# Optimization experiments

Measured on AMD Instinct MI355X. Metric: run time of the kernel, lower is better.

Reference implementation:

```python
import jax, jax.numpy as jnp
import numpy as np

EMBED_DIM = 1024
NUM_HEADS = 16
HEAD_DIM = EMBED_DIM // NUM_HEADS


def setup_inputs() -> dict:
    key = jax.random.key(0)
    k_x, k_wqkv, k_bqkv, k_wp, k_bp = jax.random.split(key, 5)
    B, N, C = 4, 2048, EMBED_DIM
    bound_qkv = 1.0 / np.sqrt(C)
    bound_p = 1.0 / np.sqrt(C)
    return {
        "x": jax.random.normal(k_x, (B, N, C), dtype=jnp.float32),
        # nn.Linear stores weight as [out, in]; we keep that layout and use x @ W.T
        "w_qkv": jax.random.uniform(k_wqkv, (3 * C, C), jnp.float32, -bound_qkv, bound_qkv),
        "b_qkv": jax.random.uniform(k_bqkv, (3 * C,), jnp.float32, -bound_qkv, bound_qkv),
        "w_proj": jax.random.uniform(k_wp, (C, C), jnp.float32, -bound_p, bound_p),
        "b_proj": jax.random.uniform(k_bp, (C,), jnp.float32, -bound_p, bound_p),
    }


def reference(x, w_qkv, b_qkv, w_proj, b_proj):
    B, N, C = x.shape
    H, D = NUM_HEADS, HEAD_DIM
    qkv = x @ w_qkv.T + b_qkv                      # [B, N, 3C]
    qkv = qkv.reshape(B, N, 3, H, D)
    q = qkv[:, :, 0].transpose(0, 2, 1, 3)          # [B, H, N, D]
    k = qkv[:, :, 1].transpose(0, 2, 1, 3)
    v = qkv[:, :, 2].transpose(0, 2, 1, 3)
    scale = jnp.asarray(D, x.dtype) ** -0.5
    attn = jnp.einsum('bhqd,bhkd->bhqk', q, k) * scale  # [B, H, N, N]
    attn = jax.nn.softmax(attn, axis=-1)
    out = jnp.einsum('bhqk,bhkd->bhqd', attn, v)        # [B, H, N, D]
    out = out.transpose(0, 2, 1, 3).reshape(B, N, C)
    return out @ w_proj.T + b_proj
```

## Files before the change

kernel.cpp:

```cpp
#include <hip/hip_runtime.h>

typedef unsigned short u16;
typedef __attribute__((ext_vector_type(8))) short short8;
typedef __attribute__((ext_vector_type(4))) short s16x4;
typedef __attribute__((ext_vector_type(8))) _Float16 half8;
typedef __attribute__((ext_vector_type(4))) float f32x4;
typedef __attribute__((ext_vector_type(16))) float f32x16;
typedef __attribute__((ext_vector_type(4))) unsigned int u32x4;

#define DEVI static __device__ __forceinline__

static constexpr int B_ = 4, N_ = 2048, C_ = 1024, H_ = 16, D_ = 64;
static constexpr int M_ = B_ * N_;
static constexpr int C3 = 3072;

DEVI u16 f2h(float f) {
  _Float16 h = (_Float16)f;
  return __builtin_bit_cast(u16, h);
}

DEVI unsigned pk2h(float lo, float hi) {
  return __builtin_bit_cast(unsigned, __builtin_amdgcn_cvt_pkrtz(lo, hi));
}

DEVI void gload_lds16(const void* g, void* lds) {
  __builtin_amdgcn_global_load_lds(
      (const __attribute__((address_space(1))) unsigned int*)g,
      (__attribute__((address_space(3))) unsigned int*)lds, 16, 0, 0);
}

__global__ __launch_bounds__(256) void f32_to_f16(const float* __restrict__ src,
                                                  u16* __restrict__ dst, int n8) {
  int idx = blockIdx.x * 256 + threadIdx.x;
  if (idx >= n8) return;
  const float* s = src + (size_t)idx * 8;
  f32x4 f0 = *(const f32x4*)s;
  f32x4 f1 = *(const f32x4*)(s + 4);
  short8 o;
#pragma unroll
  for (int j = 0; j < 8; ++j) o[j] = (short)f2h(j < 4 ? f0[j] : f1[j - 4]);
  *(short8*)(dst + (size_t)idx * 8) = o;
}

template <bool OUT_F16>
__global__ __launch_bounds__(256) void gemm_bt(const u16* __restrict__ A,
                                               const u16* __restrict__ Bm,
                                               const float* __restrict__ bias,
                                               void* __restrict__ outp, int Nout) {
  __shared__ u16 As[128 * 32];
  __shared__ u16 Bs[128 * 32];
  const int tid = threadIdx.x;
  const int w = tid >> 6, l = tid & 63;
  const int wr = w >> 1, wc = w & 1;
  const int l15 = l & 15, lg = l >> 4;
  const int nx = gridDim.x;
  int bid = blockIdx.y * nx + blockIdx.x;
  int cpx = (nx * gridDim.y) >> 3;
  int swz = (bid & 7) * cpx + (bid >> 3);
  int bx = swz % nx, by = swz / nx;
  const u16* Ab = A + (size_t)(bx * 128) * C_;
  const u16* Bb = Bm + (size_t)(by * 128) * C_;
  const int arow = tid >> 2, ac8 = (tid & 3) * 8;
  f32x4 acc[4][4];
#pragma unroll
  for (int m = 0; m < 4; ++m)
#pragma unroll
    for (int n = 0; n < 4; ++n) acc[m][n] = (f32x4){0.f, 0.f, 0.f, 0.f};

  for (int kt = 0; kt < C_; kt += 32) {
    __syncthreads();
#pragma unroll
    for (int i = 0; i < 2; ++i) {
      gload_lds16(Ab + (size_t)(i * 64 + arow) * C_ + kt + ac8,
                  (char*)As + (i * 64 + w * 16) * 64);
      gload_lds16(Bb + (size_t)(i * 64 + arow) * C_ + kt + ac8,
                  (char*)Bs + (i * 64 + w * 16) * 64);
    }
    __syncthreads();
    half8 af[4], bf[4];
#pragma unroll
    for (int m = 0; m < 4; ++m)
      af[m] = __builtin_bit_cast(half8, *(const short8*)((const char*)As +
                  (wr * 64 + m * 16 + l15) * 64 + lg * 16));
#pragma unroll
    for (int n = 0; n < 4; ++n)
      bf[n] = __builtin_bit_cast(half8, *(const short8*)((const char*)Bs +
                  (wc * 64 + n * 16 + l15) * 64 + lg * 16));
#pragma unroll
    for (int m = 0; m < 4; ++m)
#pragma unroll
      for (int n = 0; n < 4; ++n)
        acc[m][n] = __builtin_amdgcn_mfma_f32_16x16x32_f16(af[m], bf[n], acc[m][n], 0, 0, 0);
  }
#pragma unroll
  for (int m = 0; m < 4; ++m)
#pragma unroll
    for (int n = 0; n < 4; ++n) {
      int col = by * 128 + wc * 64 + n * 16 + l15;
      float bval = bias[col];
#pragma unroll
      for (int i = 0; i < 4; ++i) {
        int row = bx * 128 + wr * 64 + m * 16 + lg * 4 + i;
        float v = acc[m][n][i] + bval;
        if (OUT_F16)
          ((u16*)outp)[(size_t)row * Nout + col] = f2h(v);
        else
          ((float*)outp)[(size_t)row * Nout + col] = v;
      }
    }
}

__global__ __launch_bounds__(256) void kfrag_prep(const u16* __restrict__ qkv,
                                                  u16* __restrict__ kf) {
  int g = blockIdx.x * 256 + threadIdx.x;
  int l = g & 63;
  int df = (g >> 6) & 3;
  int kh = (g >> 8) & 1;
  int t = (g >> 9) & 31;
  int bh = g >> 14;
  int b = bh >> 4, h = bh & 15;
  const u16* src = qkv + (size_t)(b * N_ + t * 64 + kh * 32 + (l & 31)) * C3 +
                   C_ + h * D_ + (df * 2 + (l >> 5)) * 8;
  *(short8*)(kf + (size_t)g * 8) = *(const short8*)src;
}

__global__ __launch_bounds__(256) void vfrag_prep(const u16* __restrict__ qkv,
                                                  u16* __restrict__ vf) {
  __shared__ u16 tile[64][72];
  const int tid = threadIdx.x;
  const int bh = blockIdx.y, b = bh >> 4, h = bh & 15;
  const int t = blockIdx.x;
  const int r = tid >> 3, c8 = (tid & 7) * 8;
#pragma unroll
  for (int rr = 0; rr < 2; ++rr) {
    int row = rr * 32 + r;
    short8 v = *(const short8*)(qkv + (size_t)(b * N_ + t * 64 + row) * C3 +
                                2 * C_ + h * D_ + c8);
    *(short8*)&tile[row][c8] = v;
  }
  __syncthreads();
  const int l = tid & 63, wv = tid >> 6;
  const int l31 = l & 31, hi = l >> 5;
#pragma unroll
  for (int i = 0; i < 2; ++i) {
    int combo = wv * 2 + i;
    int vh = combo >> 2, kc = combo & 3;
    short8 o;
#pragma unroll
    for (int jj = 0; jj < 8; ++jj)
      o[jj] = (short)tile[kc * 16 + (jj & 3) + 8 * (jj >> 2) + 4 * hi][vh * 32 + l31];
    *(short8*)(vf + ((size_t)(bh * 32 + t) * 8 + combo) * 512 + l * 8) = o;
  }
}

__global__ __launch_bounds__(256, 2) void attn_fused(const u16* __restrict__ qkv,
                                                     const u16* __restrict__ kf,
                                                     const u16* __restrict__ vf,
                                                     u16* __restrict__ att) {
  __shared__ float red[2][64][68];
  const int tid = threadIdx.x;
  const int w = tid >> 6, l = tid & 63;
  const int l31 = l & 31, hi = l >> 5;
  const int qg = w >> 1, kvh = w & 1;
  int bid = blockIdx.y * gridDim.x + blockIdx.x;
  int swz = (bid & 7) * 128 + (bid >> 3);
  const int qt = swz & 15, bh = swz >> 4;
  const int b = bh >> 4, h = bh & 15;
  const int qb = qt * 128 + qg * 64;

  const float sc2 = 0.125f * 1.4426950408889634f;
  half8 qfA[4], qfB[4];
  {
    const _Float16 sch = (_Float16)sc2;
    const u16* qrowA = qkv + (size_t)(b * N_ + qb + l31) * C3 + h * D_ + hi * 8;
    const u16* qrowB = qrowA + (size_t)32 * C3;
#pragma unroll
    for (int df = 0; df < 4; ++df) {
      half8 qa = __builtin_bit_cast(half8, *(const short8*)(qrowA + df * 16));
      half8 qc = __builtin_bit_cast(half8, *(const short8*)(qrowB + df * 16));
#pragma unroll
      for (int j = 0; j < 8; ++j) { qa[j] *= sch; qc[j] *= sch; }
      qfA[df] = qa;
      qfB[df] = qc;
    }
  }

  f32x16 aA0, aA1, aB0, aB1;
#pragma unroll
  for (int j = 0; j < 16; ++j) { aA0[j] = 0.f; aA1[j] = 0.f; aB0[j] = 0.f; aB1[j] = 0.f; }
  float lrowA = 0.f, lrowB = 0.f;

  const u16* kp = kf + (size_t)bh * 32 * 4096;
  const u16* vp = vf + (size_t)bh * 32 * 4096;
  const int loff = l * 8;

#define MKPF(SV, J0, OUT)                                                      \
  {                                                                            \
    u32x4 wq = {pk2h(SV[J0 + 0], SV[J0 + 1]), pk2h(SV[J0 + 2], SV[J0 + 3]),   \
                pk2h(SV[J0 + 4], SV[J0 + 5]), pk2h(SV[J0 + 6], SV[J0 + 7])};   \
    OUT = __builtin_bit_cast(half8, wq);                                       \
  }

  const int t0 = kvh * 16;
  const int trot = qg * 8;
  for (int i = 0; i < 16; ++i) {
    const int t = t0 + ((i + trot) & 15);
    const u16* kt = kp + t * 4096;
    const u16* vt = vp + t * 4096;

    half8 kfr[2][4];
#pragma unroll
    for (int kh = 0; kh < 2; ++kh)
#pragma unroll
      for (int df = 0; df < 4; ++df)
        kfr[kh][df] = __builtin_bit_cast(half8,
            *(const short8*)(kt + ((kh * 4 + df) * 64) * 8 + loff));

    f32x16 sA0, sA1;
#pragma unroll
    for (int j = 0; j < 16; ++j) { sA0[j] = 0.f; sA1[j] = 0.f; }
#pragma unroll
    for (int df = 0; df < 4; ++df) {
      sA0 = __builtin_amdgcn_mfma_f32_32x32x16_f16(kfr[0][df], qfA[df], sA0, 0, 0, 0);
      sA1 = __builtin_amdgcn_mfma_f32_32x32x16_f16(kfr[1][df], qfA[df], sA1, 0, 0, 0);
    }
    float suA[4] = {0.f, 0.f, 0.f, 0.f};
#pragma unroll
    for (int j = 0; j < 16; ++j) {
      sA0[j] = __builtin_amdgcn_exp2f(sA0[j]);
      suA[j & 3] += sA0[j];
    }
#pragma unroll
    for (int j = 0; j < 16; ++j) {
      sA1[j] = __builtin_amdgcn_exp2f(sA1[j]);
      suA[j & 3] += sA1[j];
    }
    lrowA += (suA[0] + suA[1]) + (suA[2] + suA[3]);
    half8 pfA0, pfA1, pfA2, pfA3;
    MKPF(sA0, 0, pfA0)
    MKPF(sA0, 8, pfA1)
    MKPF(sA1, 0, pfA2)
    MKPF(sA1, 8, pfA3)

    f32x16 sB0, sB1;
#pragma unroll
    for (int j = 0; j < 16; ++j) { sB0[j] = 0.f; sB1[j] = 0.f; }
#pragma unroll
    for (int df = 0; df < 4; ++df) {
      sB0 = __builtin_amdgcn_mfma_f32_32x32x16_f16(kfr[0][df], qfB[df], sB0, 0, 0, 0);
      sB1 = __builtin_amdgcn_mfma_f32_32x32x16_f16(kfr[1][df], qfB[df], sB1, 0, 0, 0);
    }

    half8 vfr[2][4];
#pragma unroll
    for (int vh = 0; vh < 2; ++vh)
#pragma unroll
      for (int kc = 0; kc < 4; ++kc)
        vfr[vh][kc] = __builtin_bit_cast(half8,
            *(const short8*)(vt + ((vh * 4 + kc) * 64) * 8 + loff));

    float suB[4] = {0.f, 0.f, 0.f, 0.f};
#pragma unroll
    for (int j = 0; j < 16; ++j) {
      sB0[j] = __builtin_amdgcn_exp2f(sB0[j]);
      suB[j & 3] += sB0[j];
    }
#pragma unroll
    for (int j = 0; j < 16; ++j) {
      sB1[j] = __builtin_amdgcn_exp2f(sB1[j]);
      suB[j & 3] += sB1[j];
    }
    lrowB += (suB[0] + suB[1]) + (suB[2] + suB[3]);
    half8 pfB0, pfB1, pfB2, pfB3;
    MKPF(sB0, 0, pfB0)
    MKPF(sB0, 8, pfB1)
    MKPF(sB1, 0, pfB2)
    MKPF(sB1, 8, pfB3)

    aA0 = __builtin_amdgcn_mfma_f32_32x32x16_f16(vfr[0][0], pfA0, aA0, 0, 0, 0);
    aA1 = __builtin_amdgcn_mfma_f32_32x32x16_f16(vfr[1][0], pfA0, aA1, 0, 0, 0);
    aB0 = __builtin_amdgcn_mfma_f32_32x32x16_f16(vfr[0][0], pfB0, aB0, 0, 0, 0);
    aB1 = __builtin_amdgcn_mfma_f32_32x32x16_f16(vfr[1][0], pfB0, aB1, 0, 0, 0);
    aA0 = __builtin_amdgcn_mfma_f32_32x32x16_f16(vfr[0][1], pfA1, aA0, 0, 0, 0);
    aA1 = __builtin_amdgcn_mfma_f32_32x32x16_f16(vfr[1][1], pfA1, aA1, 0, 0, 0);
    aB0 = __builtin_amdgcn_mfma_f32_32x32x16_f16(vfr[0][1], pfB1, aB0, 0, 0, 0);
    aB1 = __builtin_amdgcn_mfma_f32_32x32x16_f16(vfr[1][1], pfB1, aB1, 0, 0, 0);
    aA0 = __builtin_amdgcn_mfma_f32_32x32x16_f16(vfr[0][2], pfA2, aA0, 0, 0, 0);
    aA1 = __builtin_amdgcn_mfma_f32_32x32x16_f16(vfr[1][2], pfA2, aA1, 0, 0, 0);
    aB0 = __builtin_amdgcn_mfma_f32_32x32x16_f16(vfr[0][2], pfB2, aB0, 0, 0, 0);
    aB1 = __builtin_amdgcn_mfma_f32_32x32x16_f16(vfr[1][2], pfB2, aB1, 0, 0, 0);
    aA0 = __builtin_amdgcn_mfma_f32_32x32x16_f16(vfr[0][3], pfA3, aA0, 0, 0, 0);
    aA1 = __builtin_amdgcn_mfma_f32_32x32x16_f16(vfr[1][3], pfA3, aA1, 0, 0, 0);
    aB0 = __builtin_amdgcn_mfma_f32_32x32x16_f16(vfr[0][3], pfB3, aB0, 0, 0, 0);
    aB1 = __builtin_amdgcn_mfma_f32_32x32x16_f16(vfr[1][3], pfB3, aB1, 0, 0, 0);
  }
#undef MKPF

  if (kvh) {
    float* s = &red[qg][l][0];
#pragma unroll
    for (int j = 0; j < 16; ++j) {
      s[j] = aA0[j];
      s[16 + j] = aA1[j];
      s[32 + j] = aB0[j];
      s[48 + j] = aB1[j];
    }
    s[64] = lrowA;
    s[65] = lrowB;
  }
  __syncthreads();
  if (!kvh) {
    const float* s = &red[qg][l][0];
#pragma unroll
    for (int j = 0; j < 16; ++j) {
      aA0[j] += s[j];
      aA1[j] += s[16 + j];
      aB0[j] += s[32 + j];
      aB1[j] += s[48 + j];
    }
    lrowA += s[64];
    lrowB += s[65];

    lrowA += __shfl_xor(lrowA, 32);
    lrowB += __shfl_xor(lrowB, 32);
    float rinvA = 1.0f / lrowA;
    float rinvB = 1.0f / lrowB;
    u16* orowA = att + (size_t)(b * N_ + qb + l31) * C_ + h * D_;
    u16* orowB = orowA + (size_t)32 * C_;
#pragma unroll
    for (int dt = 0; dt < 2; ++dt) {
#pragma unroll
      for (int r2 = 0; r2 < 4; ++r2) {
        int d0 = dt * 32 + r2 * 8 + hi * 4;
        s16x4 hvA, hvB;
#pragma unroll
        for (int i = 0; i < 4; ++i) {
          float vA = (dt ? aA1[r2 * 4 + i] : aA0[r2 * 4 + i]) * rinvA;
          float vB = (dt ? aB1[r2 * 4 + i] : aB0[r2 * 4 + i]) * rinvB;
          hvA[i] = (short)f2h(vA);
          hvB[i] = (short)f2h(vB);
        }
        *(s16x4*)(orowA + d0) = hvA;
        *(s16x4*)(orowB + d0) = hvB;
      }
    }
  }
}

extern "C" void kernel_launch(void* const* d_in, const int* in_sizes, int n_in,
                              void* d_out, int out_size, void* d_ws, size_t ws_size,
                              hipStream_t stream) {
  const float* x = (const float*)d_in[0];
  const float* w_qkv = (const float*)d_in[1];
  const float* b_qkv = (const float*)d_in[2];
  const float* w_proj = (const float*)d_in[3];
  const float* b_proj = (const float*)d_in[4];

  char* ws = (char*)d_ws;
  u16* qkv  = (u16*)(ws + 0);
  u16* x16  = (u16*)(ws + 50331648);
  u16* wq16 = (u16*)(ws + 67108864);
  u16* wp16 = (u16*)(ws + 73400320);
  u16* kf   = (u16*)(ws + 75497472);
  u16* vf   = (u16*)(ws + 92274688);
  u16* att  = (u16*)(ws + 109051904);

  f32_to_f16<<<4096, 256, 0, stream>>>(x, x16, M_ * C_ / 8);
  f32_to_f16<<<1536, 256, 0, stream>>>(w_qkv, wq16, 3 * C_ * C_ / 8);
  f32_to_f16<<<512, 256, 0, stream>>>(w_proj, wp16, C_ * C_ / 8);

  gemm_bt<true><<<dim3(64, 24), 256, 0, stream>>>(x16, wq16, b_qkv, qkv, C3);

  kfrag_prep<<<4096, 256, 0, stream>>>(qkv, kf);
  vfrag_prep<<<dim3(32, 64), 256, 0, stream>>>(qkv, vf);

  attn_fused<<<dim3(16, 64), 256, 0, stream>>>(qkv, kf, vf, att);

  gemm_bt<false><<<dim3(64, 8), 256, 0, stream>>>(att, wp16, b_proj, d_out, C_);
}
```

Measured before the change: 209.2 us.

## Triple-buffer GEMM LDS stages with async loads and larger 256x128 tiles

```diff
diff --git a/kernel.cpp b/kernel.cpp
--- a/kernel.cpp
+++ b/kernel.cpp
@@ -43,64 +43,89 @@
 }
 
 template <bool OUT_F16>
-__global__ __launch_bounds__(256) void gemm_bt(const u16* __restrict__ A,
-                                               const u16* __restrict__ Bm,
-                                               const float* __restrict__ bias,
-                                               void* __restrict__ outp, int Nout) {
-  __shared__ u16 As[128 * 32];
-  __shared__ u16 Bs[128 * 32];
+__global__ __launch_bounds__(512, 2) void gemm_bt(const u16* __restrict__ A,
+                                                  const u16* __restrict__ Bm,
+                                                  const float* __restrict__ bias,
+                                                  void* __restrict__ outp, int Nout) {
+  __shared__ u16 As[3][256 * 32];
+  __shared__ u16 Bs[3][128 * 32];
   const int tid = threadIdx.x;
   const int w = tid >> 6, l = tid & 63;
-  const int wr = w >> 1, wc = w & 1;
+  const int wr = w >> 2, wc = w & 3;
   const int l15 = l & 15, lg = l >> 4;
   const int nx = gridDim.x;
   int bid = blockIdx.y * nx + blockIdx.x;
   int cpx = (nx * gridDim.y) >> 3;
   int swz = (bid & 7) * cpx + (bid >> 3);
   int bx = swz % nx, by = swz / nx;
-  const u16* Ab = A + (size_t)(bx * 128) * C_;
+  const u16* Ab = A + (size_t)(bx * 256) * C_;
   const u16* Bb = Bm + (size_t)(by * 128) * C_;
-  const int arow = tid >> 2, ac8 = (tid & 3) * 8;
-  f32x4 acc[4][4];
-#pragma unroll
-  for (int m = 0; m < 4; ++m)
-#pragma unroll
-    for (int n = 0; n < 4; ++n) acc[m][n] = (f32x4){0.f, 0.f, 0.f, 0.f};
-
-  for (int kt = 0; kt < C_; kt += 32) {
-    __syncthreads();
+
+  f32x4 acc[8][2];
+#pragma unroll
+  for (int m = 0; m < 8; ++m)
+#pragma unroll
+    for (int n = 0; n < 2; ++n) acc[m][n] = (f32x4){0.f, 0.f, 0.f, 0.f};
+
+  auto STAGE = [&](int t, int bb) {
+    const int kt = t * 32;
 #pragma unroll
     for (int i = 0; i < 2; ++i) {
-      gload_lds16(Ab + (size_t)(i * 64 + arow) * C_ + kt + ac8,
-                  (char*)As + (i * 64 + w * 16) * 64);
-      gload_lds16(Bb + (size_t)(i * 64 + arow) * C_ + kt + ac8,
-                  (char*)Bs + (i * 64 + w * 16) * 64);
-    }
-    __syncthreads();
-    half8 af[4], bf[4];
-#pragma unroll
-    for (int m = 0; m < 4; ++m)
-      af[m] = __builtin_bit_cast(half8, *(const short8*)((const char*)As +
-                  (wr * 64 + m * 16 + l15) * 64 + lg * 16));
-#pragma unroll
-    for (int n = 0; n < 4; ++n)
-      bf[n] = __builtin_bit_cast(half8, *(const short8*)((const char*)Bs +
-                  (wc * 64 + n * 16 + l15) * 64 + lg * 16));
-#pragma unroll
-    for (int m = 0; m < 4; ++m)
-#pragma unroll
-      for (int n = 0; n < 4; ++n)
+      const int c = i * 512 + tid;
+      gload_lds16(Ab + (size_t)(c >> 2) * C_ + kt + (c & 3) * 8,
+                  (char*)&As[bb][0] + (i * 512 + w * 64) * 16);
+    }
+    gload_lds16(Bb + (size_t)(tid >> 2) * C_ + kt + (tid & 3) * 8,
+                (char*)&Bs[bb][0] + (w * 64) * 16);
+  };
+
+  STAGE(0, 0);
+  STAGE(1, 1);
+  asm volatile("s_waitcnt vmcnt(3)" ::: "memory");
+  __builtin_amdgcn_sched_barrier(0);
+  __builtin_amdgcn_s_barrier();
+  __builtin_amdgcn_sched_barrier(0);
+
+  for (int t = 0; t < 32; ++t) {
+    const int cur = t % 3;
+    if (t + 2 < 32) STAGE(t + 2, (t + 2) % 3);
+    const char* Ablk = (const char*)&As[cur][0];
+    const char* Bblk = (const char*)&Bs[cur][0];
+    half8 bf[2];
+#pragma unroll
+    for (int n = 0; n < 2; ++n)
+      bf[n] = __builtin_bit_cast(half8, *(const short8*)(Bblk +
+                  (wc * 32 + n * 16 + l15) * 64 + lg * 16));
+    half8 af[8];
+#pragma unroll
+    for (int m = 0; m < 8; ++m)
+      af[m] = __builtin_bit_cast(half8, *(const short8*)(Ablk +
+                  (wr * 128 + m * 16 + l15) * 64 + lg * 16));
+#pragma unroll
+    for (int m = 0; m < 8; ++m)
+#pragma unroll
+      for (int n = 0; n < 2; ++n)
         acc[m][n] = __builtin_amdgcn_mfma_f32_16x16x32_f16(af[m], bf[n], acc[m][n], 0, 0, 0);
-  }
-#pragma unroll
-  for (int m = 0; m < 4; ++m)
-#pragma unroll
-    for (int n = 0; n < 4; ++n) {
-      int col = by * 128 + wc * 64 + n * 16 + l15;
+    if (t + 1 < 32) {
+      if (t + 2 < 32)
+        asm volatile("s_waitcnt vmcnt(3)" ::: "memory");
+      else
+        asm volatile("s_waitcnt vmcnt(0)" ::: "memory");
+      __builtin_amdgcn_sched_barrier(0);
+      __builtin_amdgcn_s_barrier();
+      __builtin_amdgcn_sched_barrier(0);
+    }
+  }
+
+#pragma unroll
+  for (int m = 0; m < 8; ++m)
+#pragma unroll
+    for (int n = 0; n < 2; ++n) {
+      int col = by * 128 + wc * 32 + n * 16 + l15;
       float bval = bias[col];
 #pragma unroll
       for (int i = 0; i < 4; ++i) {
-        int row = bx * 128 + wr * 64 + m * 16 + lg * 4 + i;
+        int row = bx * 256 + wr * 128 + m * 16 + lg * 4 + i;
         float v = acc[m][n][i] + bval;
         if (OUT_F16)
           ((u16*)outp)[(size_t)row * Nout + col] = f2h(v);
@@ -369,12 +394,12 @@
   f32_to_f16<<<1536, 256, 0, stream>>>(w_qkv, wq16, 3 * C_ * C_ / 8);
   f32_to_f16<<<512, 256, 0, stream>>>(w_proj, wp16, C_ * C_ / 8);
 
-  gemm_bt<true><<<dim3(64, 24), 256, 0, stream>>>(x16, wq16, b_qkv, qkv, C3);
+  gemm_bt<true><<<dim3(32, 24), 512, 0, stream>>>(x16, wq16, b_qkv, qkv, C3);
 
   kfrag_prep<<<4096, 256, 0, stream>>>(qkv, kf);
   vfrag_prep<<<dim3(32, 64), 256, 0, stream>>>(qkv, vf);
 
   attn_fused<<<dim3(16, 64), 256, 0, stream>>>(qkv, kf, vf, att);
 
-  gemm_bt<false><<<dim3(64, 8), 256, 0, stream>>>(att, wp16, b_proj, d_out, C_);
-}
+  gemm_bt<false><<<dim3(32, 8), 512, 0, stream>>>(att, wp16, b_proj, d_out, C_);
+}
```

New measurement: 243.3 us. 16.3% more time.

## Double GEMM K-tile with XOR-swizzled LDS and merge small prep kernels

Applied to the files above, without the earlier changes.

```diff
diff --git a/kernel.cpp b/kernel.cpp
--- a/kernel.cpp
+++ b/kernel.cpp
@@ -29,17 +29,30 @@
       (__attribute__((address_space(3))) unsigned int*)lds, 16, 0, 0);
 }
 
-__global__ __launch_bounds__(256) void f32_to_f16(const float* __restrict__ src,
-                                                  u16* __restrict__ dst, int n8) {
+__global__ __launch_bounds__(256) void f32_to_f16_all(const float* __restrict__ x,
+                                                      const float* __restrict__ wq,
+                                                      const float* __restrict__ wp,
+                                                      u16* __restrict__ x16,
+                                                      u16* __restrict__ wq16,
+                                                      u16* __restrict__ wp16) {
   int idx = blockIdx.x * 256 + threadIdx.x;
-  if (idx >= n8) return;
-  const float* s = src + (size_t)idx * 8;
-  f32x4 f0 = *(const f32x4*)s;
-  f32x4 f1 = *(const f32x4*)(s + 4);
+  const float* s;
+  u16* d;
+  int base;
+  if (idx < 1048576) {
+    s = x; d = x16; base = idx;
+  } else if (idx < 1048576 + 393216) {
+    s = wq; d = wq16; base = idx - 1048576;
+  } else {
+    s = wp; d = wp16; base = idx - 1441792;
+  }
+  const float* sp = s + (size_t)base * 8;
+  f32x4 f0 = *(const f32x4*)sp;
+  f32x4 f1 = *(const f32x4*)(sp + 4);
   short8 o;
 #pragma unroll
   for (int j = 0; j < 8; ++j) o[j] = (short)f2h(j < 4 ? f0[j] : f1[j - 4]);
-  *(short8*)(dst + (size_t)idx * 8) = o;
+  *(short8*)(d + (size_t)base * 8) = o;
 }
 
 template <bool OUT_F16>
@@ -47,12 +60,13 @@
                                                const u16* __restrict__ Bm,
                                                const float* __restrict__ bias,
                                                void* __restrict__ outp, int Nout) {
-  __shared__ u16 As[128 * 32];
-  __shared__ u16 Bs[128 * 32];
+  __shared__ u16 As[128 * 64];
+  __shared__ u16 Bs[128 * 64];
   const int tid = threadIdx.x;
   const int w = tid >> 6, l = tid & 63;
   const int wr = w >> 1, wc = w & 1;
   const int l15 = l & 15, lg = l >> 4;
+  const int e7 = l15 & 7;
   const int nx = gridDim.x;
   int bid = blockIdx.y * nx + blockIdx.x;
   int cpx = (nx * gridDim.y) >> 3;
@@ -60,37 +74,43 @@
   int bx = swz % nx, by = swz / nx;
   const u16* Ab = A + (size_t)(bx * 128) * C_;
   const u16* Bb = Bm + (size_t)(by * 128) * C_;
-  const int arow = tid >> 2, ac8 = (tid & 3) * 8;
+  const int srow = tid >> 3;
+  const int sgc8 = (((tid & 7) ^ ((tid >> 3) & 7)) * 8);
+  const int fc0 = (lg ^ e7) << 4;
+  const int fc1 = ((4 + lg) ^ e7) << 4;
   f32x4 acc[4][4];
 #pragma unroll
   for (int m = 0; m < 4; ++m)
 #pragma unroll
     for (int n = 0; n < 4; ++n) acc[m][n] = (f32x4){0.f, 0.f, 0.f, 0.f};
 
-  for (int kt = 0; kt < C_; kt += 32) {
+  for (int kt = 0; kt < C_; kt += 64) {
     __syncthreads();
 #pragma unroll
-    for (int i = 0; i < 2; ++i) {
-      gload_lds16(Ab + (size_t)(i * 64 + arow) * C_ + kt + ac8,
-                  (char*)As + (i * 64 + w * 16) * 64);
-      gload_lds16(Bb + (size_t)(i * 64 + arow) * C_ + kt + ac8,
-                  (char*)Bs + (i * 64 + w * 16) * 64);
+    for (int i = 0; i < 4; ++i) {
+      int r = i * 32 + srow;
+      gload_lds16(Ab + (size_t)r * C_ + kt + sgc8, (char*)As + i * 4096 + w * 1024);
+      gload_lds16(Bb + (size_t)r * C_ + kt + sgc8, (char*)Bs + i * 4096 + w * 1024);
     }
     __syncthreads();
-    half8 af[4], bf[4];
-#pragma unroll
-    for (int m = 0; m < 4; ++m)
-      af[m] = __builtin_bit_cast(half8, *(const short8*)((const char*)As +
-                  (wr * 64 + m * 16 + l15) * 64 + lg * 16));
-#pragma unroll
-    for (int n = 0; n < 4; ++n)
-      bf[n] = __builtin_bit_cast(half8, *(const short8*)((const char*)Bs +
-                  (wc * 64 + n * 16 + l15) * 64 + lg * 16));
-#pragma unroll
-    for (int m = 0; m < 4; ++m)
+#pragma unroll
+    for (int kk = 0; kk < 2; ++kk) {
+      const int fco = kk ? fc1 : fc0;
+      half8 af[4], bf[4];
+#pragma unroll
+      for (int m = 0; m < 4; ++m)
+        af[m] = __builtin_bit_cast(half8, *(const short8*)((const char*)As +
+                    (wr * 64 + m * 16 + l15) * 128 + fco));
 #pragma unroll
       for (int n = 0; n < 4; ++n)
-        acc[m][n] = __builtin_amdgcn_mfma_f32_16x16x32_f16(af[m], bf[n], acc[m][n], 0, 0, 0);
+        bf[n] = __builtin_bit_cast(half8, *(const short8*)((const char*)Bs +
+                    (wc * 64 + n * 16 + l15) * 128 + fco));
+#pragma unroll
+      for (int m = 0; m < 4; ++m)
+#pragma unroll
+        for (int n = 0; n < 4; ++n)
+          acc[m][n] = __builtin_amdgcn_mfma_f32_16x16x32_f16(af[m], bf[n], acc[m][n], 0, 0, 0);
+    }
   }
 #pragma unroll
   for (int m = 0; m < 4; ++m)
@@ -110,26 +130,28 @@
     }
 }
 
-__global__ __launch_bounds__(256) void kfrag_prep(const u16* __restrict__ qkv,
-                                                  u16* __restrict__ kf) {
-  int g = blockIdx.x * 256 + threadIdx.x;
-  int l = g & 63;
-  int df = (g >> 6) & 3;
-  int kh = (g >> 8) & 1;
-  int t = (g >> 9) & 31;
-  int bh = g >> 14;
-  int b = bh >> 4, h = bh & 15;
-  const u16* src = qkv + (size_t)(b * N_ + t * 64 + kh * 32 + (l & 31)) * C3 +
-                   C_ + h * D_ + (df * 2 + (l >> 5)) * 8;
-  *(short8*)(kf + (size_t)g * 8) = *(const short8*)src;
-}
-
-__global__ __launch_bounds__(256) void vfrag_prep(const u16* __restrict__ qkv,
-                                                  u16* __restrict__ vf) {
+__global__ __launch_bounds__(256) void kv_prep(const u16* __restrict__ qkv,
+                                               u16* __restrict__ kf,
+                                               u16* __restrict__ vf) {
   __shared__ u16 tile[64][72];
+  const int bxk = blockIdx.x;
+  if (bxk < 4096) {
+    int g = bxk * 256 + threadIdx.x;
+    int l = g & 63;
+    int df = (g >> 6) & 3;
+    int kh = (g >> 8) & 1;
+    int t = (g >> 9) & 31;
+    int bh = g >> 14;
+    int b = bh >> 4, h = bh & 15;
+    const u16* src = qkv + (size_t)(b * N_ + t * 64 + kh * 32 + (l & 31)) * C3 +
+                     C_ + h * D_ + (df * 2 + (l >> 5)) * 8;
+    *(short8*)(kf + (size_t)g * 8) = *(const short8*)src;
+    return;
+  }
+  const int idx2 = bxk - 4096;
+  const int t = idx2 & 31, bh = idx2 >> 5;
+  const int b = bh >> 4, h = bh & 15;
   const int tid = threadIdx.x;
-  const int bh = blockIdx.y, b = bh >> 4, h = bh & 15;
-  const int t = blockIdx.x;
   const int r = tid >> 3, c8 = (tid & 7) * 8;
 #pragma unroll
   for (int rr = 0; rr < 2; ++rr) {
@@ -365,14 +387,11 @@
   u16* vf   = (u16*)(ws + 92274688);
   u16* att  = (u16*)(ws + 109051904);
 
-  f32_to_f16<<<4096, 256, 0, stream>>>(x, x16, M_ * C_ / 8);
-  f32_to_f16<<<1536, 256, 0, stream>>>(w_qkv, wq16, 3 * C_ * C_ / 8);
-  f32_to_f16<<<512, 256, 0, stream>>>(w_proj, wp16, C_ * C_ / 8);
+  f32_to_f16_all<<<6144, 256, 0, stream>>>(x, w_qkv, w_proj, x16, wq16, wp16);
 
   gemm_bt<true><<<dim3(64, 24), 256, 0, stream>>>(x16, wq16, b_qkv, qkv, C3);
 
-  kfrag_prep<<<4096, 256, 0, stream>>>(qkv, kf);
-  vfrag_prep<<<dim3(32, 64), 256, 0, stream>>>(qkv, vf);
+  kv_prep<<<6144, 256, 0, stream>>>(qkv, kf, vf);
 
   attn_fused<<<dim3(16, 64), 256, 0, stream>>>(qkv, kf, vf, att);
 
```

Measured after the change: 201.4 us. -3.7%, faster.
